# Kernel tuning notes

Measured on AMD Instinct MI355X. Metric: run time of the kernel, lower is better.

The kernel has to match this reference:

```python
import jax, jax.numpy as jnp
import numpy as np

BIG = 1e9  # self-distance masking constant, as in the torch module


def setup_inputs() -> dict:
    key = jax.random.key(0)
    k1, _ = jax.random.split(key)
    coords = jax.random.normal(k1, (8, 4096, 3), dtype=jnp.float32)
    mask = jnp.ones((8, 4096), dtype=bool)
    return {"coords": coords, "mask": mask}


def reference(coords, mask):
    # coords: [B, N, 3]; mask is accepted but unused (matches the torch module)
    B, N, _ = coords.shape
    # Pairwise Euclidean distances via the |a|^2 + |b|^2 - 2ab identity
    # (avoids materializing the [B,N,N,3] diff tensor the torch code builds).
    sq = jnp.sum(coords * coords, axis=-1)                      # [B, N]
    inner = jnp.einsum('bnd,bmd->bnm', coords, coords)          # [B, N, N]
    d2 = sq[:, :, None] + sq[:, None, :] - 2.0 * inner
    dist = jnp.sqrt(jnp.maximum(d2, 0.0))                       # [B, N, N]
    dist = dist + jnp.eye(N, dtype=dist.dtype) * BIG            # mask self
    # argsort(dim=2)[:, :, :2] == indices of the two smallest distances
    _, idx = jax.lax.top_k(-dist, 2)                            # [B, N, 2]
    first_nearest_indices = idx[:, :, 0]
    second_nearest_indices = idx[:, :, 1]
    A = jnp.take_along_axis(
        coords, jnp.broadcast_to(first_nearest_indices[:, :, None], (B, N, 3)), axis=1)
    C = jnp.take_along_axis(
        coords, jnp.broadcast_to(second_nearest_indices[:, :, None], (B, N, 3)), axis=1)
    return (A, C, first_nearest_indices, second_nearest_indices)
```

## Files before the change

kernel.cpp:

```cpp
#include <hip/hip_runtime.h>

#define BATCH 8
#define NPTS 4096
#define TOTQ (BATCH * NPTS)
#define TPB 256
#define BIGD 1e30f

__device__ __forceinline__ void top2min(float k, int m,
                                        float& b1, int& i1,
                                        float& b2, int& i2) {
    bool c1 = k < b1;
    bool c2 = k < b2;
    int ni2 = c2 ? m : i2;
    i2 = c1 ? i1 : ni2;
    i1 = c1 ? m : i1;
    b2 = fminf(fmaxf(k, b1), b2);
    b1 = fminf(k, b1);
}

template <int CHUNKSZ, int Q, bool EXC>
__device__ __forceinline__ void scan_loop(const float4* __restrict__ pts, int mbase,
                                          const int* nq,
                                          const float* xn, const float* yn, const float* zn,
                                          float* b1, int* i1, float* b2, int* i2) {
    for (int p = 0; p < CHUNKSZ; p += 4) {
        float4 c[4];
#pragma unroll
        for (int j = 0; j < 4; ++j) c[j] = pts[p + j];
#pragma unroll
        for (int j = 0; j < 4; ++j) {
            const int m = mbase + p + j;
#pragma unroll
            for (int q = 0; q < Q; ++q) {
                float k = fmaf(c[j].x, xn[q], fmaf(c[j].y, yn[q], fmaf(c[j].z, zn[q], c[j].w)));
                if (EXC) k = (m == nq[q]) ? BIGD : k;
                top2min(k, m, b1[q], i1[q], b2[q], i2[q]);
            }
        }
    }
}

template <int NCHUNKS, int Q>
__global__ __launch_bounds__(TPB, 4) void knn_scan(const float* __restrict__ coords,
                                                   float4* __restrict__ partial) {
    constexpr int CHUNKSZ = NPTS / NCHUNKS;
    __shared__ float4 pts[CHUNKSZ];
    const int tid   = (int)threadIdx.x;
    const int tile  = blockIdx.x;
    const int chunk = blockIdx.y;
    const int b     = blockIdx.z;
    const float* basep = coords + (size_t)b * NPTS * 3;
    const int mbase = chunk * CHUNKSZ;

    for (int p = tid; p < CHUNKSZ; p += TPB) {
        float x = basep[(mbase + p) * 3 + 0];
        float y = basep[(mbase + p) * 3 + 1];
        float z = basep[(mbase + p) * 3 + 2];
        pts[p] = make_float4(-2.0f * x, -2.0f * y, -2.0f * z,
                             fmaf(x, x, fmaf(y, y, z * z)));
    }

    const int qbase = tile * (TPB * Q);
    int nq[Q];
    float xn[Q], yn[Q], zn[Q], b1[Q], b2[Q];
    int i1[Q], i2[Q];
#pragma unroll
    for (int q = 0; q < Q; ++q) {
        int n = qbase + q * TPB + tid;
        nq[q] = n;
        xn[q] = basep[n * 3 + 0];
        yn[q] = basep[n * 3 + 1];
        zn[q] = basep[n * 3 + 2];
        b1[q] = BIGD; b2[q] = BIGD; i1[q] = 0; i2[q] = 0;
    }
    __syncthreads();

    const int qend = qbase + TPB * Q;
    const int mend = mbase + CHUNKSZ;
    if (mbase < qend && qbase < mend) {
        scan_loop<CHUNKSZ, Q, true >(pts, mbase, nq, xn, yn, zn, b1, i1, b2, i2);
    } else {
        scan_loop<CHUNKSZ, Q, false>(pts, mbase, nq, xn, yn, zn, b1, i1, b2, i2);
    }

#pragma unroll
    for (int q = 0; q < Q; ++q) {
        int n = qbase + q * TPB + tid;
        partial[(size_t)chunk * TOTQ + (size_t)b * NPTS + n] =
            make_float4(b1[q], __int_as_float(i1[q]), b2[q], __int_as_float(i2[q]));
    }
}

template <int NCHUNKS>
__global__ __launch_bounds__(TPB) void knn_merge(const float* __restrict__ coords,
                                                 const float4* __restrict__ partial,
                                                 float* __restrict__ out) {
    const int q = blockIdx.x * TPB + (int)threadIdx.x;
    const int b = q >> 12;
    float b1 = BIGD, b2 = BIGD;
    int i1 = 0, i2 = 0;
#pragma unroll 8
    for (int c = 0; c < NCHUNKS; ++c) {
        float4 pc = partial[(size_t)c * TOTQ + q];
        top2min(pc.x, __float_as_int(pc.y), b1, i1, b2, i2);
        top2min(pc.z, __float_as_int(pc.w), b1, i1, b2, i2);
    }
    const float* basep = coords + (size_t)b * NPTS * 3;
    float* A  = out;
    float* C  = out + (size_t)TOTQ * 3;
    float* I1 = out + (size_t)2 * TOTQ * 3;
    float* I2 = I1 + (size_t)TOTQ;

    A[(size_t)q * 3 + 0] = basep[i1 * 3 + 0];
    A[(size_t)q * 3 + 1] = basep[i1 * 3 + 1];
    A[(size_t)q * 3 + 2] = basep[i1 * 3 + 2];
    C[(size_t)q * 3 + 0] = basep[i2 * 3 + 0];
    C[(size_t)q * 3 + 1] = basep[i2 * 3 + 1];
    C[(size_t)q * 3 + 2] = basep[i2 * 3 + 2];
    I1[q] = (float)i1;
    I2[q] = (float)i2;
}

__global__ __launch_bounds__(TPB) void knn_full(const float* __restrict__ coords,
                                                float* __restrict__ out) {
    __shared__ float4 pts[NPTS];
    const int tid  = (int)threadIdx.x;
    const int tile = blockIdx.x;
    const int b    = blockIdx.y;
    const float* basep = coords + (size_t)b * NPTS * 3;

    for (int p = tid; p < NPTS; p += TPB) {
        float x = basep[p * 3 + 0];
        float y = basep[p * 3 + 1];
        float z = basep[p * 3 + 2];
        pts[p] = make_float4(-2.0f * x, -2.0f * y, -2.0f * z,
                             fmaf(x, x, fmaf(y, y, z * z)));
    }
    const int n = tile * TPB + tid;
    const float xn = basep[n * 3 + 0];
    const float yn = basep[n * 3 + 1];
    const float zn = basep[n * 3 + 2];
    __syncthreads();

    float b1 = BIGD, b2 = BIGD;
    int i1 = 0, i2 = 0;
    for (int p = 0; p < NPTS; p += 4) {
#pragma unroll
        for (int j = 0; j < 4; ++j) {
            float4 c = pts[p + j];
            float k = fmaf(c.x, xn, fmaf(c.y, yn, fmaf(c.z, zn, c.w)));
            k = (p + j == n) ? BIGD : k;
            top2min(k, p + j, b1, i1, b2, i2);
        }
    }

    const int q = b * NPTS + n;
    float* A  = out;
    float* C  = out + (size_t)TOTQ * 3;
    float* I1 = out + (size_t)2 * TOTQ * 3;
    float* I2 = I1 + (size_t)TOTQ;
    float4 p1 = pts[i1];
    float4 p2 = pts[i2];
    A[(size_t)q * 3 + 0] = -0.5f * p1.x;
    A[(size_t)q * 3 + 1] = -0.5f * p1.y;
    A[(size_t)q * 3 + 2] = -0.5f * p1.z;
    C[(size_t)q * 3 + 0] = -0.5f * p2.x;
    C[(size_t)q * 3 + 1] = -0.5f * p2.y;
    C[(size_t)q * 3 + 2] = -0.5f * p2.z;
    I1[q] = (float)i1;
    I2[q] = (float)i2;
}

extern "C" void kernel_launch(void* const* d_in, const int* in_sizes, int n_in,
                              void* d_out, int out_size, void* d_ws, size_t ws_size,
                              hipStream_t stream) {
    const float* coords = (const float*)d_in[0];
    float* out = (float*)d_out;
    float4* partial = (float4*)d_ws;
    const size_t chunk_bytes = (size_t)TOTQ * sizeof(float4);

    if (ws_size >= 64 * chunk_bytes) {
        hipLaunchKernelGGL((knn_scan<64, 8>), dim3(2, 64, BATCH), dim3(TPB), 0, stream,
                           coords, partial);
        hipLaunchKernelGGL((knn_merge<64>), dim3(TOTQ / TPB), dim3(TPB), 0, stream,
                           coords, partial, out);
    } else if (ws_size >= 32 * chunk_bytes) {
        hipLaunchKernelGGL((knn_scan<32, 8>), dim3(2, 32, BATCH), dim3(TPB), 0, stream,
                           coords, partial);
        hipLaunchKernelGGL((knn_merge<32>), dim3(TOTQ / TPB), dim3(TPB), 0, stream,
                           coords, partial, out);
    } else {
        hipLaunchKernelGGL(knn_full, dim3(NPTS / TPB, BATCH), dim3(TPB), 0, stream,
                           coords, out);
    }
}
```

Baseline: 113.1 us.

## Scan chunk minima without indices, then resolve neighbors by rescanning candidate chunks

The scan kernel now tracks only the two smallest key values per 64-point chunk, dropping index tracking and the self-exclusion test. This halves the partial-result storage and removes the index selects from the hot loop. The merge kernel picks the two best chunks plus the query's own chunk, then rescans those chunks with one lane per point and a wave shuffle reduction to recover exact indices with lexicographic tie-breaking. In exchange, the merge stage does extra recomputation and more synchronisation.

```diff
diff --git a/kernel.cpp b/kernel.cpp
--- a/kernel.cpp
+++ b/kernel.cpp
@@ -4,7 +4,184 @@
 #define NPTS 4096
 #define TOTQ (BATCH * NPTS)
 #define TPB 256
+#define NCH 64
+#define CSZ 64
+#define QF 8
 #define BIGD 1e30f
+#define MAXI 0x7fffffff
+
+__device__ __forceinline__ float cand_w(float x, float y, float z) {
+    return fmaf(x, x, fmaf(y, y, z * z));
+}
+__device__ __forceinline__ float cand_key(float cx, float cy, float cz, float w,
+                                          float xn, float yn, float zn) {
+    return fmaf(cx, xn, fmaf(cy, yn, fmaf(cz, zn, w)));
+}
+
+__device__ __forceinline__ void lexup(float k, int i,
+                                      float& b1, int& i1,
+                                      float& b2, int& i2) {
+    bool c1 = (k < b1) || (k == b1 && i < i1);
+    bool c2 = (k < b2) || (k == b2 && i < i2);
+    float nb2 = c1 ? b1 : (c2 ? k : b2);
+    int   ni2 = c1 ? i1 : (c2 ? i : i2);
+    b1 = c1 ? k : b1;
+    i1 = c1 ? i : i1;
+    b2 = nb2;
+    i2 = ni2;
+}
+
+__global__ __launch_bounds__(TPB) void knn_scan_v(const float* __restrict__ coords,
+                                                  float2* __restrict__ vals) {
+    __shared__ float4 pts[CSZ];
+    const int tid   = (int)threadIdx.x;
+    const int tile  = blockIdx.x;
+    const int chunk = blockIdx.y;
+    const int b     = blockIdx.z;
+    const float* basep = coords + (size_t)b * NPTS * 3;
+    const int mbase = chunk * CSZ;
+
+    if (tid < CSZ) {
+        float x = basep[(mbase + tid) * 3 + 0];
+        float y = basep[(mbase + tid) * 3 + 1];
+        float z = basep[(mbase + tid) * 3 + 2];
+        pts[tid] = make_float4(-2.0f * x, -2.0f * y, -2.0f * z, cand_w(x, y, z));
+    }
+
+    const int qbase = tile * (TPB * QF);
+    float xn[QF], yn[QF], zn[QF], b1[QF], b2[QF];
+#pragma unroll
+    for (int q = 0; q < QF; ++q) {
+        int n = qbase + q * TPB + tid;
+        xn[q] = basep[n * 3 + 0];
+        yn[q] = basep[n * 3 + 1];
+        zn[q] = basep[n * 3 + 2];
+        b1[q] = BIGD; b2[q] = BIGD;
+    }
+    __syncthreads();
+
+    for (int p = 0; p < CSZ; p += 4) {
+        float4 c[4];
+#pragma unroll
+        for (int j = 0; j < 4; ++j) c[j] = pts[p + j];
+#pragma unroll
+        for (int j = 0; j < 4; ++j) {
+#pragma unroll
+            for (int q = 0; q < QF; ++q) {
+                float k = cand_key(c[j].x, c[j].y, c[j].z, c[j].w, xn[q], yn[q], zn[q]);
+                b2[q] = fminf(fmaxf(k, b1[q]), b2[q]);
+                b1[q] = fminf(k, b1[q]);
+            }
+        }
+    }
+
+#pragma unroll
+    for (int q = 0; q < QF; ++q) {
+        int n = qbase + q * TPB + tid;
+        vals[(size_t)chunk * TOTQ + (size_t)b * NPTS + n] = make_float2(b1[q], b2[q]);
+    }
+}
+
+__global__ __launch_bounds__(TPB) void knn_merge_w(const float* __restrict__ coords,
+                                                   const float2* __restrict__ vals,
+                                                   float* __restrict__ out) {
+    __shared__ float4 part[4][CSZ];
+    __shared__ int4 rl[CSZ];
+    __shared__ int2 res[CSZ];
+    const int t  = (int)threadIdx.x;
+    const int qi = t & 63;
+    const int s  = t >> 6;
+    const int qb = blockIdx.x * 64;
+    const int q  = qb + qi;
+    const int b  = qb >> 12;
+    const int c_self = (qb & (NPTS - 1)) >> 6;
+    const float* bp = coords + (size_t)b * NPTS * 3;
+
+    float f1 = BIGD, f2 = BIGD;
+    int t1 = MAXI, t2 = MAXI;
+    for (int c = s * 16; c < s * 16 + 16; ++c) {
+        if (c == c_self) continue;
+        float2 v = vals[(size_t)c * TOTQ + q];
+        lexup(v.x, 2 * c + 0, f1, t1, f2, t2);
+        lexup(v.y, 2 * c + 1, f1, t1, f2, t2);
+    }
+    part[s][qi] = make_float4(f1, __int_as_float(t1), f2, __int_as_float(t2));
+    __syncthreads();
+
+    if (s == 0) {
+#pragma unroll
+        for (int ss = 1; ss < 4; ++ss) {
+            float4 p = part[ss][qi];
+            lexup(p.x, __float_as_int(p.y), f1, t1, f2, t2);
+            lexup(p.z, __float_as_int(p.w), f1, t1, f2, t2);
+        }
+        const int ca = t1 >> 1;
+        const int cb = t2 >> 1;
+        const int lo = min(min(ca, cb), c_self);
+        const int hi = max(max(ca, cb), c_self);
+        const int md = ca + cb + c_self - lo - hi;
+        rl[qi] = make_int4(lo, md, hi, 0);
+    }
+    __syncthreads();
+
+    const int lane = qi;
+    const int w = s;
+    for (int j = 0; j < 16; ++j) {
+        const int qj = w * 16 + j;
+        const int4 r = rl[qj];
+        const int n = (qb + qj) & (NPTS - 1);
+        const float xq = bp[n * 3 + 0];
+        const float yq = bp[n * 3 + 1];
+        const float zq = bp[n * 3 + 2];
+
+        float b1 = BIGD, b2 = BIGD;
+        int i1 = MAXI, i2 = MAXI;
+        int prev = -1;
+#pragma unroll
+        for (int u = 0; u < 3; ++u) {
+            const int c = (u == 0) ? r.x : (u == 1) ? r.y : r.z;
+            if (c == prev) continue;
+            prev = c;
+            const int m = c * CSZ + lane;
+            const float x = bp[m * 3 + 0];
+            const float y = bp[m * 3 + 1];
+            const float z = bp[m * 3 + 2];
+            const float wv = cand_w(x, y, z);
+            float k = cand_key(-2.0f * x, -2.0f * y, -2.0f * z, wv, xq, yq, zq);
+            const bool self = (m == n);
+            k = self ? BIGD : k;
+            lexup(k, self ? MAXI : m, b1, i1, b2, i2);
+        }
+#pragma unroll
+        for (int off = 1; off < 64; off <<= 1) {
+            const float ok1 = __shfl_xor(b1, off);
+            const int   oi1 = __shfl_xor(i1, off);
+            const float ok2 = __shfl_xor(b2, off);
+            const int   oi2 = __shfl_xor(i2, off);
+            lexup(ok1, oi1, b1, i1, b2, i2);
+            lexup(ok2, oi2, b1, i1, b2, i2);
+        }
+        if (lane == 0) res[qj] = make_int2(i1, i2);
+    }
+    __syncthreads();
+
+    if (s == 0) {
+        const int i1 = res[qi].x;
+        const int i2 = res[qi].y;
+        float* A  = out;
+        float* C  = out + (size_t)TOTQ * 3;
+        float* I1 = out + (size_t)2 * TOTQ * 3;
+        float* I2 = I1 + (size_t)TOTQ;
+        A[(size_t)q * 3 + 0] = bp[i1 * 3 + 0];
+        A[(size_t)q * 3 + 1] = bp[i1 * 3 + 1];
+        A[(size_t)q * 3 + 2] = bp[i1 * 3 + 2];
+        C[(size_t)q * 3 + 0] = bp[i2 * 3 + 0];
+        C[(size_t)q * 3 + 1] = bp[i2 * 3 + 1];
+        C[(size_t)q * 3 + 2] = bp[i2 * 3 + 2];
+        I1[q] = (float)i1;
+        I2[q] = (float)i2;
+    }
+}
 
 __device__ __forceinline__ void top2min(float k, int m,
                                         float& b1, int& i1,
@@ -18,109 +195,6 @@
     b1 = fminf(k, b1);
 }
 
-template <int CHUNKSZ, int Q, bool EXC>
-__device__ __forceinline__ void scan_loop(const float4* __restrict__ pts, int mbase,
-                                          const int* nq,
-                                          const float* xn, const float* yn, const float* zn,
-                                          float* b1, int* i1, float* b2, int* i2) {
-    for (int p = 0; p < CHUNKSZ; p += 4) {
-        float4 c[4];
-#pragma unroll
-        for (int j = 0; j < 4; ++j) c[j] = pts[p + j];
-#pragma unroll
-        for (int j = 0; j < 4; ++j) {
-            const int m = mbase + p + j;
-#pragma unroll
-            for (int q = 0; q < Q; ++q) {
-                float k = fmaf(c[j].x, xn[q], fmaf(c[j].y, yn[q], fmaf(c[j].z, zn[q], c[j].w)));
-                if (EXC) k = (m == nq[q]) ? BIGD : k;
-                top2min(k, m, b1[q], i1[q], b2[q], i2[q]);
-            }
-        }
-    }
-}
-
-template <int NCHUNKS, int Q>
-__global__ __launch_bounds__(TPB, 4) void knn_scan(const float* __restrict__ coords,
-                                                   float4* __restrict__ partial) {
-    constexpr int CHUNKSZ = NPTS / NCHUNKS;
-    __shared__ float4 pts[CHUNKSZ];
-    const int tid   = (int)threadIdx.x;
-    const int tile  = blockIdx.x;
-    const int chunk = blockIdx.y;
-    const int b     = blockIdx.z;
-    const float* basep = coords + (size_t)b * NPTS * 3;
-    const int mbase = chunk * CHUNKSZ;
-
-    for (int p = tid; p < CHUNKSZ; p += TPB) {
-        float x = basep[(mbase + p) * 3 + 0];
-        float y = basep[(mbase + p) * 3 + 1];
-        float z = basep[(mbase + p) * 3 + 2];
-        pts[p] = make_float4(-2.0f * x, -2.0f * y, -2.0f * z,
-                             fmaf(x, x, fmaf(y, y, z * z)));
-    }
-
-    const int qbase = tile * (TPB * Q);
-    int nq[Q];
-    float xn[Q], yn[Q], zn[Q], b1[Q], b2[Q];
-    int i1[Q], i2[Q];
-#pragma unroll
-    for (int q = 0; q < Q; ++q) {
-        int n = qbase + q * TPB + tid;
-        nq[q] = n;
-        xn[q] = basep[n * 3 + 0];
-        yn[q] = basep[n * 3 + 1];
-        zn[q] = basep[n * 3 + 2];
-        b1[q] = BIGD; b2[q] = BIGD; i1[q] = 0; i2[q] = 0;
-    }
-    __syncthreads();
-
-    const int qend = qbase + TPB * Q;
-    const int mend = mbase + CHUNKSZ;
-    if (mbase < qend && qbase < mend) {
-        scan_loop<CHUNKSZ, Q, true >(pts, mbase, nq, xn, yn, zn, b1, i1, b2, i2);
-    } else {
-        scan_loop<CHUNKSZ, Q, false>(pts, mbase, nq, xn, yn, zn, b1, i1, b2, i2);
-    }
-
-#pragma unroll
-    for (int q = 0; q < Q; ++q) {
-        int n = qbase + q * TPB + tid;
-        partial[(size_t)chunk * TOTQ + (size_t)b * NPTS + n] =
-            make_float4(b1[q], __int_as_float(i1[q]), b2[q], __int_as_float(i2[q]));
-    }
-}
-
-template <int NCHUNKS>
-__global__ __launch_bounds__(TPB) void knn_merge(const float* __restrict__ coords,
-                                                 const float4* __restrict__ partial,
-                                                 float* __restrict__ out) {
-    const int q = blockIdx.x * TPB + (int)threadIdx.x;
-    const int b = q >> 12;
-    float b1 = BIGD, b2 = BIGD;
-    int i1 = 0, i2 = 0;
-#pragma unroll 8
-    for (int c = 0; c < NCHUNKS; ++c) {
-        float4 pc = partial[(size_t)c * TOTQ + q];
-        top2min(pc.x, __float_as_int(pc.y), b1, i1, b2, i2);
-        top2min(pc.z, __float_as_int(pc.w), b1, i1, b2, i2);
-    }
-    const float* basep = coords + (size_t)b * NPTS * 3;
-    float* A  = out;
-    float* C  = out + (size_t)TOTQ * 3;
-    float* I1 = out + (size_t)2 * TOTQ * 3;
-    float* I2 = I1 + (size_t)TOTQ;
-
-    A[(size_t)q * 3 + 0] = basep[i1 * 3 + 0];
-    A[(size_t)q * 3 + 1] = basep[i1 * 3 + 1];
-    A[(size_t)q * 3 + 2] = basep[i1 * 3 + 2];
-    C[(size_t)q * 3 + 0] = basep[i2 * 3 + 0];
-    C[(size_t)q * 3 + 1] = basep[i2 * 3 + 1];
-    C[(size_t)q * 3 + 2] = basep[i2 * 3 + 2];
-    I1[q] = (float)i1;
-    I2[q] = (float)i2;
-}
-
 __global__ __launch_bounds__(TPB) void knn_full(const float* __restrict__ coords,
                                                 float* __restrict__ out) {
     __shared__ float4 pts[NPTS];
@@ -133,8 +207,7 @@
         float x = basep[p * 3 + 0];
         float y = basep[p * 3 + 1];
         float z = basep[p * 3 + 2];
-        pts[p] = make_float4(-2.0f * x, -2.0f * y, -2.0f * z,
-                             fmaf(x, x, fmaf(y, y, z * z)));
+        pts[p] = make_float4(-2.0f * x, -2.0f * y, -2.0f * z, cand_w(x, y, z));
     }
     const int n = tile * TPB + tid;
     const float xn = basep[n * 3 + 0];
@@ -148,7 +221,7 @@
 #pragma unroll
         for (int j = 0; j < 4; ++j) {
             float4 c = pts[p + j];
-            float k = fmaf(c.x, xn, fmaf(c.y, yn, fmaf(c.z, zn, c.w)));
+            float k = cand_key(c.x, c.y, c.z, c.w, xn, yn, zn);
             k = (p + j == n) ? BIGD : k;
             top2min(k, p + j, b1, i1, b2, i2);
         }
@@ -176,19 +249,14 @@
                               hipStream_t stream) {
     const float* coords = (const float*)d_in[0];
     float* out = (float*)d_out;
-    float4* partial = (float4*)d_ws;
-    const size_t chunk_bytes = (size_t)TOTQ * sizeof(float4);
-
-    if (ws_size >= 64 * chunk_bytes) {
-        hipLaunchKernelGGL((knn_scan<64, 8>), dim3(2, 64, BATCH), dim3(TPB), 0, stream,
-                           coords, partial);
-        hipLaunchKernelGGL((knn_merge<64>), dim3(TOTQ / TPB), dim3(TPB), 0, stream,
-                           coords, partial, out);
-    } else if (ws_size >= 32 * chunk_bytes) {
-        hipLaunchKernelGGL((knn_scan<32, 8>), dim3(2, 32, BATCH), dim3(TPB), 0, stream,
-                           coords, partial);
-        hipLaunchKernelGGL((knn_merge<32>), dim3(TOTQ / TPB), dim3(TPB), 0, stream,
-                           coords, partial, out);
+
+    const size_t need = (size_t)NCH * TOTQ * sizeof(float2);
+    if (ws_size >= need) {
+        float2* vals = (float2*)d_ws;
+        hipLaunchKernelGGL(knn_scan_v, dim3(NPTS / (TPB * QF), NCH, BATCH), dim3(TPB),
+                           0, stream, coords, vals);
+        hipLaunchKernelGGL(knn_merge_w, dim3(TOTQ / 64), dim3(TPB), 0, stream,
+                           coords, vals, out);
     } else {
         hipLaunchKernelGGL(knn_full, dim3(NPTS / TPB, BATCH), dim3(TPB), 0, stream,
                            coords, out);
```

After: 123.9 us. 9.5% more time.
